# Kernel tuning notes

Measured on AMD Instinct MI355X. Metric: run time of the kernel, lower is better.

The kernel has to match this reference:

```python
import jax, jax.numpy as jnp
import numpy as np
from jax import lax

B, T, C = 4, 2048, 1024
E, DFF, TOPK = 8, 4096, 2


def setup_inputs() -> dict:
    key = jax.random.key(0)
    ks = jax.random.split(key, 5)
    scale = 0.02
    x = jax.random.normal(ks[0], (B, T, C), dtype=jnp.float32)
    router_w = jax.random.normal(ks[1], (C, E), dtype=jnp.float32) * scale
    router_b = jnp.zeros((E,), dtype=jnp.float32)
    w1 = jax.random.normal(ks[2], (E, C, DFF), dtype=jnp.float32) * scale
    b1 = jnp.zeros((E, DFF), dtype=jnp.float32)
    w2 = jax.random.normal(ks[3], (E, DFF, C), dtype=jnp.float32) * scale
    b2 = jnp.zeros((E, C), dtype=jnp.float32)
    return {"x": x, "router_w": router_w, "router_b": router_b,
            "w1": w1, "b1": b1, "w2": w2, "b2": b2, "top_k": TOPK}


def reference(x, router_w, router_b, w1, b1, w2, b2, top_k):
    # Router: softmax then top-k (matches torch.topk(F.softmax(logits)))
    logits = jnp.einsum('btc,ce->bte', x, router_w) + router_b   # [B,T,E]
    probs = jax.nn.softmax(logits, axis=-1)
    weights, indices = lax.top_k(probs, top_k)                    # [B,T,k]
    n_exp = w1.shape[0]
    # Combined per-expert weight per token (sum over top-k slots hitting expert j)
    onehot = jax.nn.one_hot(indices, n_exp, dtype=x.dtype)        # [B,T,k,E]
    cw = jnp.sum(weights[..., None] * onehot, axis=-2)            # [B,T,E]
    bsz, seq, dim = x.shape
    flat_x = x.reshape(-1, dim)                                   # [N,C]
    flat_cw = cw.reshape(-1, n_exp)                               # [N,E]
    out = jnp.zeros_like(flat_x)
    for j in range(n_exp):  # fixed small expert loop (dropout=0 -> eval)
        h = jax.nn.gelu(flat_x @ w1[j] + b1[j], approximate=False)
        out = out + flat_cw[:, j:j + 1] * (h @ w2[j] + b2[j])
    return out.reshape(bsz, seq, dim)
```

## Files before the change

### kernel.cpp

```cpp
#include <hip/hip_runtime.h>
#include <math.h>

typedef __bf16 bf16;
typedef bf16 bf16x4 __attribute__((ext_vector_type(4)));
typedef bf16 bf16x8 __attribute__((ext_vector_type(8)));
typedef float f32x4 __attribute__((ext_vector_type(4)));

#define NTOK 8192
#define CDIM 1024
#define EXP 8
#define DFF 4096
#define BM 256
#define BN 256
#define BK 64

__device__ __forceinline__ void gld_lds16(const bf16* g, bf16* l) {
  __builtin_amdgcn_global_load_lds(
      (const __attribute__((address_space(1))) unsigned int*)g,
      (__attribute__((address_space(3))) unsigned int*)l, 16, 0, 0);
}

__global__ __launch_bounds__(256) void convert_x(const float* __restrict__ in,
                                                 bf16* __restrict__ out) {
  int idx = (blockIdx.x * 256 + threadIdx.x) * 8;
  float4 a = *(const float4*)(in + idx);
  float4 b = *(const float4*)(in + idx + 4);
  bf16x8 v;
  v[0] = (bf16)a.x; v[1] = (bf16)a.y; v[2] = (bf16)a.z; v[3] = (bf16)a.w;
  v[4] = (bf16)b.x; v[5] = (bf16)b.y; v[6] = (bf16)b.z; v[7] = (bf16)b.w;
  *(bf16x8*)(out + idx) = v;
}

__global__ __launch_bounds__(256) void transpose_cvt(
    const float* __restrict__ in, bf16* __restrict__ out, int R, int Cin) {
  __shared__ float tile[32][33];
  int e = blockIdx.z;
  const float* ip = in + (size_t)e * R * Cin;
  bf16* op = out + (size_t)e * R * Cin;
  int c0 = blockIdx.x * 32, r0 = blockIdx.y * 32;
  int tx = threadIdx.x & 31, ty = threadIdx.x >> 5;
#pragma unroll
  for (int i = 0; i < 4; i++)
    tile[ty + 8 * i][tx] = ip[(size_t)(r0 + ty + 8 * i) * Cin + c0 + tx];
  __syncthreads();
  int c = threadIdx.x >> 3, r4 = (threadIdx.x & 7) * 4;
  bf16x4 v;
  v[0] = (bf16)tile[r4][c];
  v[1] = (bf16)tile[r4 + 1][c];
  v[2] = (bf16)tile[r4 + 2][c];
  v[3] = (bf16)tile[r4 + 3][c];
  *(bf16x4*)&op[(size_t)(c0 + c) * R + r0 + r4] = v;
}

__global__ __launch_bounds__(256) void router_kernel(
    const float* __restrict__ x, const float* __restrict__ rw,
    const float* __restrict__ rb, unsigned int* __restrict__ cnt,
    int* __restrict__ list, float* __restrict__ wq) {
  int wave = threadIdx.x >> 6, lane = threadIdx.x & 63;
  int t = blockIdx.x * 4 + wave;
  if (t >= NTOK) return;
  const float* xr = x + (size_t)t * CDIM;
  float acc[8] = {0.f, 0.f, 0.f, 0.f, 0.f, 0.f, 0.f, 0.f};
  for (int c = lane; c < CDIM; c += 64) {
    float xv = xr[c];
    const float4* rp = (const float4*)(rw + c * 8);
    float4 r0 = rp[0], r1 = rp[1];
    acc[0] += xv * r0.x; acc[1] += xv * r0.y;
    acc[2] += xv * r0.z; acc[3] += xv * r0.w;
    acc[4] += xv * r1.x; acc[5] += xv * r1.y;
    acc[6] += xv * r1.z; acc[7] += xv * r1.w;
  }
#pragma unroll
  for (int e = 0; e < 8; e++)
#pragma unroll
    for (int off = 32; off; off >>= 1) acc[e] += __shfl_down(acc[e], off);
  if (lane == 0) {
    float p[8], mx = -1e30f;
#pragma unroll
    for (int e = 0; e < 8; e++) { p[e] = acc[e] + rb[e]; mx = fmaxf(mx, p[e]); }
    float s = 0.f;
#pragma unroll
    for (int e = 0; e < 8; e++) { p[e] = expf(p[e] - mx); s += p[e]; }
    float inv = 1.0f / s;
#pragma unroll
    for (int e = 0; e < 8; e++) p[e] *= inv;
    int i1 = 0;
#pragma unroll
    for (int e = 1; e < 8; e++) if (p[e] > p[i1]) i1 = e;
    int i2 = (i1 == 0) ? 1 : 0;
#pragma unroll
    for (int e = 0; e < 8; e++) if (e != i1 && p[e] > p[i2]) i2 = e;
    unsigned s0 = atomicAdd(&cnt[i1], 1u);
    list[i1 * NTOK + s0] = t * 2;
    unsigned s1 = atomicAdd(&cnt[i2], 1u);
    list[i2 * NTOK + s1] = t * 2 + 1;
    wq[t * 2] = p[i1];
    wq[t * 2 + 1] = p[i2];
  }
}

__global__ __launch_bounds__(512, 2) void gemm1_kernel(
    const bf16* __restrict__ xb, const bf16* __restrict__ w1b,
    const float* __restrict__ b1, const int* __restrict__ list,
    const unsigned int* __restrict__ cnt, bf16* __restrict__ h) {
  int bid = blockIdx.x + 16 * (blockIdx.y + 32 * blockIdx.z);
  int wg = (bid & 7) * 512 + (bid >> 3);
  int n0 = (wg & 15) * BN;
  int mt = (wg >> 4) & 31;
  int e = wg >> 9;
  int count = (int)min(cnt[e], (unsigned)NTOK);
  int m0 = mt * BM;
  if (m0 >= count) return;

  __shared__ __align__(16) bf16 As[BM][BK];
  __shared__ __align__(16) bf16 Bs[BN][BK];

  int tid = threadIdx.x;
  int w = tid >> 6, l = tid & 63;
  int lhi = l >> 3, llo = l & 7;
  int w8l = w * 8 + lhi;
  int dst8 = llo * 8;
  int sc8 = (llo ^ lhi) * 8;

  const int* lp = list + e * NTOK;
  const bf16* aptr[4];
  const bf16* bptr[4];
#pragma unroll
  for (int p = 0; p < 4; p++) {
    int row = p * 64 + w8l;
    int enc = lp[min(m0 + row, count - 1)];
    aptr[p] = xb + (size_t)(enc >> 1) * CDIM + sc8;
    bptr[p] = w1b + (size_t)e * DFF * CDIM + (size_t)(n0 + row) * CDIM + sc8;
  }

  f32x4 acc[8][4] = {};
  int wm = w >> 2, wn = w & 3;
  int ln = l & 15, kq = l >> 4;
  int rx = ln & 7;

  for (int k0 = 0; k0 < CDIM; k0 += BK) {
    __syncthreads();
#pragma unroll
    for (int p = 0; p < 4; p++) {
      gld_lds16(aptr[p] + k0, &As[p * 64 + w8l][dst8]);
      gld_lds16(bptr[p] + k0, &Bs[p * 64 + w8l][dst8]);
    }
    __syncthreads();
#pragma unroll
    for (int hh = 0; hh < 2; hh++) {
      int co = ((hh * 4 + kq) ^ rx) * 8;
      bf16x8 af[8], bfr[4];
#pragma unroll
      for (int j = 0; j < 4; j++)
        bfr[j] = *(bf16x8*)&Bs[wn * 64 + j * 16 + ln][co];
#pragma unroll
      for (int i = 0; i < 8; i++)
        af[i] = *(bf16x8*)&As[wm * 128 + i * 16 + ln][co];
#pragma unroll
      for (int i = 0; i < 8; i++)
#pragma unroll
        for (int j = 0; j < 4; j++)
          acc[i][j] = __builtin_amdgcn_mfma_f32_16x16x32_bf16(
              af[i], bfr[j], acc[i][j], 0, 0, 0);
    }
  }

  float b1f[4];
#pragma unroll
  for (int j = 0; j < 4; j++)
    b1f[j] = b1[e * DFF + n0 + wn * 64 + j * 16 + ln];
#pragma unroll
  for (int i = 0; i < 8; i++) {
#pragma unroll
    for (int r = 0; r < 4; r++) {
      int mrow = wm * 128 + i * 16 + kq * 4 + r;
      if (m0 + mrow < count) {
        int enc = lp[m0 + mrow];
        bf16* hr = h + (size_t)enc * DFF + n0 + wn * 64 + ln;
#pragma unroll
        for (int j = 0; j < 4; j++) {
          float v = acc[i][j][r] + b1f[j];
          float g = 0.5f * v * (1.0f + erff(v * 0.70710678118654752f));
          hr[j * 16] = (bf16)g;
        }
      }
    }
  }
}

__global__ __launch_bounds__(512, 2) void gemm2_kernel(
    const bf16* __restrict__ h, const bf16* __restrict__ w2b,
    const float* __restrict__ b2, const int* __restrict__ list,
    const unsigned int* __restrict__ cnt, const float* __restrict__ wq,
    float* __restrict__ out) {
  int bid = blockIdx.x + 4 * (blockIdx.y + 32 * blockIdx.z);
  int wg = (bid & 7) * 128 + (bid >> 3);
  int n0 = (wg & 3) * BN;
  int mt = (wg >> 2) & 31;
  int e = wg >> 7;
  int count = (int)min(cnt[e], (unsigned)NTOK);
  int m0 = mt * BM;
  if (m0 >= count) return;

  __shared__ __align__(16) bf16 As[BM][BK];
  __shared__ __align__(16) bf16 Bs[BN][BK];

  int tid = threadIdx.x;
  int w = tid >> 6, l = tid & 63;
  int lhi = l >> 3, llo = l & 7;
  int w8l = w * 8 + lhi;
  int dst8 = llo * 8;
  int sc8 = (llo ^ lhi) * 8;

  const int* lp = list + e * NTOK;
  const bf16* aptr[4];
  const bf16* bptr[4];
#pragma unroll
  for (int p = 0; p < 4; p++) {
    int row = p * 64 + w8l;
    int enc = lp[min(m0 + row, count - 1)];
    aptr[p] = h + (size_t)enc * DFF + sc8;
    bptr[p] = w2b + (size_t)e * CDIM * DFF + (size_t)(n0 + row) * DFF + sc8;
  }

  f32x4 acc[8][4] = {};
  int wm = w >> 2, wn = w & 3;
  int ln = l & 15, kq = l >> 4;
  int rx = ln & 7;

  for (int k0 = 0; k0 < DFF; k0 += BK) {
    __syncthreads();
#pragma unroll
    for (int p = 0; p < 4; p++) {
      gld_lds16(aptr[p] + k0, &As[p * 64 + w8l][dst8]);
      gld_lds16(bptr[p] + k0, &Bs[p * 64 + w8l][dst8]);
    }
    __syncthreads();
#pragma unroll
    for (int hh = 0; hh < 2; hh++) {
      int co = ((hh * 4 + kq) ^ rx) * 8;
      bf16x8 af[8], bfr[4];
#pragma unroll
      for (int j = 0; j < 4; j++)
        bfr[j] = *(bf16x8*)&Bs[wn * 64 + j * 16 + ln][co];
#pragma unroll
      for (int i = 0; i < 8; i++)
        af[i] = *(bf16x8*)&As[wm * 128 + i * 16 + ln][co];
#pragma unroll
      for (int i = 0; i < 8; i++)
#pragma unroll
        for (int j = 0; j < 4; j++)
          acc[i][j] = __builtin_amdgcn_mfma_f32_16x16x32_bf16(
              af[i], bfr[j], acc[i][j], 0, 0, 0);
    }
  }

  float b2f[4];
#pragma unroll
  for (int j = 0; j < 4; j++)
    b2f[j] = b2[e * CDIM + n0 + wn * 64 + j * 16 + ln];
#pragma unroll
  for (int i = 0; i < 8; i++) {
#pragma unroll
    for (int r = 0; r < 4; r++) {
      int mrow = wm * 128 + i * 16 + kq * 4 + r;
      if (m0 + mrow < count) {
        int enc = lp[m0 + mrow];
        int t = enc >> 1;
        float wt = wq[enc];
        float* orow = out + (size_t)t * CDIM + n0 + wn * 64 + ln;
#pragma unroll
        for (int j = 0; j < 4; j++)
          atomicAdd(&orow[j * 16], wt * (acc[i][j][r] + b2f[j]));
      }
    }
  }
}

extern "C" void kernel_launch(void* const* d_in, const int* in_sizes, int n_in,
                              void* d_out, int out_size, void* d_ws,
                              size_t ws_size, hipStream_t stream) {
  const float* x = (const float*)d_in[0];
  const float* rw = (const float*)d_in[1];
  const float* rb = (const float*)d_in[2];
  const float* w1 = (const float*)d_in[3];
  const float* b1 = (const float*)d_in[4];
  const float* w2 = (const float*)d_in[5];
  const float* b2 = (const float*)d_in[6];
  float* out = (float*)d_out;

  char* ws = (char*)d_ws;
  size_t o = 0;
  auto carve = [&](size_t bytes) {
    void* p = ws + o;
    o = (o + bytes + 255) & ~(size_t)255;
    return p;
  };
  bf16* w1b = (bf16*)carve((size_t)EXP * DFF * CDIM * 2);
  bf16* w2b = (bf16*)carve((size_t)EXP * DFF * CDIM * 2);
  bf16* h = (bf16*)carve((size_t)2 * NTOK * DFF * 2);
  bf16* xb = (bf16*)carve((size_t)NTOK * CDIM * 2);
  int* list = (int*)carve((size_t)EXP * NTOK * 4);
  float* wq = (float*)carve((size_t)2 * NTOK * 4);
  unsigned int* cnt = (unsigned int*)carve(64);

  hipMemsetAsync(out, 0, (size_t)out_size * sizeof(float), stream);
  hipMemsetAsync(cnt, 0, 64, stream);

  convert_x<<<NTOK * CDIM / (256 * 8), 256, 0, stream>>>(x, xb);
  transpose_cvt<<<dim3(DFF / 32, CDIM / 32, EXP), 256, 0, stream>>>(w1, w1b,
                                                                    CDIM, DFF);
  transpose_cvt<<<dim3(CDIM / 32, DFF / 32, EXP), 256, 0, stream>>>(w2, w2b,
                                                                    DFF, CDIM);
  router_kernel<<<NTOK / 4, 256, 0, stream>>>(x, rw, rb, cnt, list, wq);
  gemm1_kernel<<<dim3(DFF / BN, NTOK / BM, EXP), 512, 0, stream>>>(
      xb, w1b, b1, list, cnt, h);
  gemm2_kernel<<<dim3(CDIM / BN, NTOK / BM, EXP), 512, 0, stream>>>(
      h, w2b, b2, list, cnt, wq, out);
}
```

Before: 1.202 ms.

## Pipeline grouped GEMM core with double-buffered LDS and replace atomics with combine

Replaces the two-sync GEMM main loop with a shared gemm_core that double-buffers LDS in half-K stages, issues global-to-LDS prefetches ahead of the MFMA blocks, and raises wave priority around the MFMAs, so memory latency overlaps compute. GEMM2 now writes each routed slot's weighted result to a scratch buffer (aliased onto w1b) instead of atomically adding into the output, and a new combine kernel sums the two slots per token; this also drops the output memset. The transpose kernel now handles 64-row tiles and writes 8-element vectors. The pipeline uses 128 KB of LDS per block, which may cap occupancy below the launch bound of two blocks, and the extra scratch write plus combine pass add memory traffic.

Measured after the change: 1.086 ms. 1.11x faster.

```diff
diff --git a/kernel.cpp b/kernel.cpp
--- a/kernel.cpp
+++ b/kernel.cpp
@@ -13,6 +13,7 @@
 #define BM 256
 #define BN 256
 #define BK 64
+#define HALF_E 8192
 
 __device__ __forceinline__ void gld_lds16(const bf16* g, bf16* l) {
   __builtin_amdgcn_global_load_lds(
@@ -33,23 +34,22 @@
 
 __global__ __launch_bounds__(256) void transpose_cvt(
     const float* __restrict__ in, bf16* __restrict__ out, int R, int Cin) {
-  __shared__ float tile[32][33];
+  __shared__ float tile[64][33];
   int e = blockIdx.z;
   const float* ip = in + (size_t)e * R * Cin;
   bf16* op = out + (size_t)e * R * Cin;
-  int c0 = blockIdx.x * 32, r0 = blockIdx.y * 32;
-  int tx = threadIdx.x & 31, ty = threadIdx.x >> 5;
-#pragma unroll
-  for (int i = 0; i < 4; i++)
-    tile[ty + 8 * i][tx] = ip[(size_t)(r0 + ty + 8 * i) * Cin + c0 + tx];
+  int c0 = blockIdx.x * 32, r0 = blockIdx.y * 64;
+  int tr = threadIdx.x >> 5, tc = threadIdx.x & 31;
+#pragma unroll
+  for (int i = 0; i < 8; i++)
+    tile[tr + 8 * i][tc] = ip[(size_t)(r0 + tr + 8 * i) * Cin + c0 + tc];
   __syncthreads();
-  int c = threadIdx.x >> 3, r4 = (threadIdx.x & 7) * 4;
-  bf16x4 v;
-  v[0] = (bf16)tile[r4][c];
-  v[1] = (bf16)tile[r4 + 1][c];
-  v[2] = (bf16)tile[r4 + 2][c];
-  v[3] = (bf16)tile[r4 + 3][c];
-  *(bf16x4*)&op[(size_t)(c0 + c) * R + r0 + r4] = v;
+  int oc = threadIdx.x >> 3;
+  int orr = (threadIdx.x & 7) * 8;
+  bf16x8 v;
+#pragma unroll
+  for (int k = 0; k < 8; k++) v[k] = (bf16)tile[orr + k][oc];
+  *(bf16x8*)&op[(size_t)(c0 + oc) * R + r0 + orr] = v;
 }
 
 __global__ __launch_bounds__(256) void router_kernel(
@@ -99,6 +99,108 @@
   }
 }
 
+__device__ __forceinline__ void ld_afrag(const bf16* base, int aoff, int ih,
+                                         bf16x8 (&af)[4]) {
+#pragma unroll
+  for (int i = 0; i < 4; i++)
+    af[i] = *(const bf16x8*)&base[aoff + (ih * 64 + i * 16) * 32];
+}
+__device__ __forceinline__ void ld_bfrag(const bf16* base, int boff,
+                                         bf16x8 (&bfr)[4]) {
+#pragma unroll
+  for (int j = 0; j < 4; j++)
+    bfr[j] = *(const bf16x8*)&base[boff + j * 16 * 32];
+}
+
+#define MFMA16(IH)                                                        \
+  do {                                                                    \
+    __builtin_amdgcn_s_setprio(1);                                        \
+    _Pragma("unroll") for (int i = 0; i < 4; i++)                         \
+        _Pragma("unroll") for (int j = 0; j < 4; j++) acc[(IH)*4 + i][j] = \
+            __builtin_amdgcn_mfma_f32_16x16x32_bf16(af[i], bfr[j],        \
+                                                    acc[(IH)*4 + i][j],   \
+                                                    0, 0, 0);             \
+    __builtin_amdgcn_s_setprio(0);                                        \
+  } while (0)
+
+#define STAGE(P1, P2, LDSBUF, TK, KS)                                     \
+  do {                                                                    \
+    int _k = (TK) * BK + (KS)*32;                                         \
+    bf16* _d = &LDSBUF[(((((TK)&1) << 1) | (KS)) * HALF_E) + tid * 8];    \
+    gld_lds16((P1) + _k, _d);                                             \
+    gld_lds16((P2) + _k, _d + 4096);                                      \
+  } while (0)
+
+template <int NT>
+__device__ __forceinline__ void gemm_core(
+    const bf16* aRow1, const bf16* aRow2, const bf16* bRow1, const bf16* bRow2,
+    bf16* Asf, bf16* Bsf, int tid, f32x4 (&acc)[8][4]) {
+  int w = tid >> 6, l = tid & 63;
+  int ln = l & 15, kq = l >> 4;
+  int wm = w >> 2, wn = w & 3;
+  int rc8 = (kq ^ ((ln >> 1) & 3)) * 8;
+  int aoff = (wm * 128 + ln) * 32 + rc8;
+  int boff = (wn * 64 + ln) * 32 + rc8;
+
+  bf16x8 af[4], bfr[4];
+
+  STAGE(aRow1, aRow2, Asf, 0, 0);
+  STAGE(bRow1, bRow2, Bsf, 0, 0);
+  STAGE(aRow1, aRow2, Asf, 0, 1);
+  STAGE(bRow1, bRow2, Bsf, 0, 1);
+  STAGE(aRow1, aRow2, Asf, 1, 0);
+  STAGE(bRow1, bRow2, Bsf, 1, 0);
+  asm volatile("s_waitcnt vmcnt(8)" ::: "memory");
+  __builtin_amdgcn_s_barrier();
+
+  for (int t = 0; t < NT; ++t) {
+    int sel = (t & 1) << 1;
+    const bf16* A0 = &Asf[sel * HALF_E];
+    const bf16* A1 = &Asf[(sel | 1) * HALF_E];
+    const bf16* B0 = &Bsf[sel * HALF_E];
+    const bf16* B1 = &Bsf[(sel | 1) * HALF_E];
+
+    ld_bfrag(B0, boff, bfr);
+    ld_afrag(A0, aoff, 0, af);
+    if (t + 1 < NT) STAGE(aRow1, aRow2, Asf, t + 1, 1);
+    if (t < NT - 1) asm volatile("s_waitcnt vmcnt(6)" ::: "memory");
+    else            asm volatile("s_waitcnt vmcnt(0)" ::: "memory");
+    __builtin_amdgcn_s_barrier();
+    asm volatile("s_waitcnt lgkmcnt(0)" ::: "memory");
+    __builtin_amdgcn_sched_barrier(0);
+    MFMA16(0);
+    __builtin_amdgcn_s_barrier();
+
+    ld_afrag(A0, aoff, 1, af);
+    if (t + 1 < NT) STAGE(bRow1, bRow2, Bsf, t + 1, 1);
+    __builtin_amdgcn_s_barrier();
+    asm volatile("s_waitcnt lgkmcnt(0)" ::: "memory");
+    __builtin_amdgcn_sched_barrier(0);
+    MFMA16(1);
+    __builtin_amdgcn_s_barrier();
+
+    ld_bfrag(B1, boff, bfr);
+    ld_afrag(A1, aoff, 0, af);
+    if (t + 2 < NT) STAGE(aRow1, aRow2, Asf, t + 2, 0);
+    if (t < NT - 2)       asm volatile("s_waitcnt vmcnt(6)" ::: "memory");
+    else if (t == NT - 2) asm volatile("s_waitcnt vmcnt(2)" ::: "memory");
+    else                  asm volatile("s_waitcnt vmcnt(0)" ::: "memory");
+    __builtin_amdgcn_s_barrier();
+    asm volatile("s_waitcnt lgkmcnt(0)" ::: "memory");
+    __builtin_amdgcn_sched_barrier(0);
+    MFMA16(0);
+    __builtin_amdgcn_s_barrier();
+
+    ld_afrag(A1, aoff, 1, af);
+    if (t + 2 < NT) STAGE(bRow1, bRow2, Bsf, t + 2, 0);
+    __builtin_amdgcn_s_barrier();
+    asm volatile("s_waitcnt lgkmcnt(0)" ::: "memory");
+    __builtin_amdgcn_sched_barrier(0);
+    MFMA16(1);
+    __builtin_amdgcn_s_barrier();
+  }
+}
+
 __global__ __launch_bounds__(512, 2) void gemm1_kernel(
     const bf16* __restrict__ xb, const bf16* __restrict__ w1b,
     const float* __restrict__ b1, const int* __restrict__ list,
@@ -112,59 +214,28 @@
   int m0 = mt * BM;
   if (m0 >= count) return;
 
-  __shared__ __align__(16) bf16 As[BM][BK];
-  __shared__ __align__(16) bf16 Bs[BN][BK];
+  __shared__ __align__(16) bf16 Asf[4 * HALF_E];
+  __shared__ __align__(16) bf16 Bsf[4 * HALF_E];
 
   int tid = threadIdx.x;
+  int row1 = tid >> 2;
+  int cx8 = ((tid & 3) ^ ((tid >> 3) & 3)) * 8;
+
+  const int* lp = list + e * NTOK;
+  int encA1 = lp[min(m0 + row1, count - 1)];
+  int encA2 = lp[min(m0 + row1 + 128, count - 1)];
+  const bf16* aRow1 = xb + (size_t)(encA1 >> 1) * CDIM + cx8;
+  const bf16* aRow2 = xb + (size_t)(encA2 >> 1) * CDIM + cx8;
+  const bf16* bRow1 =
+      w1b + (size_t)e * DFF * CDIM + (size_t)(n0 + row1) * CDIM + cx8;
+  const bf16* bRow2 = bRow1 + (size_t)128 * CDIM;
+
+  f32x4 acc[8][4] = {};
+  gemm_core<CDIM / BK>(aRow1, aRow2, bRow1, bRow2, Asf, Bsf, tid, acc);
+
   int w = tid >> 6, l = tid & 63;
-  int lhi = l >> 3, llo = l & 7;
-  int w8l = w * 8 + lhi;
-  int dst8 = llo * 8;
-  int sc8 = (llo ^ lhi) * 8;
-
-  const int* lp = list + e * NTOK;
-  const bf16* aptr[4];
-  const bf16* bptr[4];
-#pragma unroll
-  for (int p = 0; p < 4; p++) {
-    int row = p * 64 + w8l;
-    int enc = lp[min(m0 + row, count - 1)];
-    aptr[p] = xb + (size_t)(enc >> 1) * CDIM + sc8;
-    bptr[p] = w1b + (size_t)e * DFF * CDIM + (size_t)(n0 + row) * CDIM + sc8;
-  }
-
-  f32x4 acc[8][4] = {};
+  int ln = l & 15, kq = l >> 4;
   int wm = w >> 2, wn = w & 3;
-  int ln = l & 15, kq = l >> 4;
-  int rx = ln & 7;
-
-  for (int k0 = 0; k0 < CDIM; k0 += BK) {
-    __syncthreads();
-#pragma unroll
-    for (int p = 0; p < 4; p++) {
-      gld_lds16(aptr[p] + k0, &As[p * 64 + w8l][dst8]);
-      gld_lds16(bptr[p] + k0, &Bs[p * 64 + w8l][dst8]);
-    }
-    __syncthreads();
-#pragma unroll
-    for (int hh = 0; hh < 2; hh++) {
-      int co = ((hh * 4 + kq) ^ rx) * 8;
-      bf16x8 af[8], bfr[4];
-#pragma unroll
-      for (int j = 0; j < 4; j++)
-        bfr[j] = *(bf16x8*)&Bs[wn * 64 + j * 16 + ln][co];
-#pragma unroll
-      for (int i = 0; i < 8; i++)
-        af[i] = *(bf16x8*)&As[wm * 128 + i * 16 + ln][co];
-#pragma unroll
-      for (int i = 0; i < 8; i++)
-#pragma unroll
-        for (int j = 0; j < 4; j++)
-          acc[i][j] = __builtin_amdgcn_mfma_f32_16x16x32_bf16(
-              af[i], bfr[j], acc[i][j], 0, 0, 0);
-    }
-  }
-
   float b1f[4];
 #pragma unroll
   for (int j = 0; j < 4; j++)
@@ -192,7 +263,7 @@
     const bf16* __restrict__ h, const bf16* __restrict__ w2b,
     const float* __restrict__ b2, const int* __restrict__ list,
     const unsigned int* __restrict__ cnt, const float* __restrict__ wq,
-    float* __restrict__ out) {
+    float* __restrict__ y) {
   int bid = blockIdx.x + 4 * (blockIdx.y + 32 * blockIdx.z);
   int wg = (bid & 7) * 128 + (bid >> 3);
   int n0 = (wg & 3) * BN;
@@ -202,59 +273,28 @@
   int m0 = mt * BM;
   if (m0 >= count) return;
 
-  __shared__ __align__(16) bf16 As[BM][BK];
-  __shared__ __align__(16) bf16 Bs[BN][BK];
+  __shared__ __align__(16) bf16 Asf[4 * HALF_E];
+  __shared__ __align__(16) bf16 Bsf[4 * HALF_E];
 
   int tid = threadIdx.x;
+  int row1 = tid >> 2;
+  int cx8 = ((tid & 3) ^ ((tid >> 3) & 3)) * 8;
+
+  const int* lp = list + e * NTOK;
+  int encA1 = lp[min(m0 + row1, count - 1)];
+  int encA2 = lp[min(m0 + row1 + 128, count - 1)];
+  const bf16* aRow1 = h + (size_t)encA1 * DFF + cx8;
+  const bf16* aRow2 = h + (size_t)encA2 * DFF + cx8;
+  const bf16* bRow1 =
+      w2b + (size_t)e * CDIM * DFF + (size_t)(n0 + row1) * DFF + cx8;
+  const bf16* bRow2 = bRow1 + (size_t)128 * DFF;
+
+  f32x4 acc[8][4] = {};
+  gemm_core<DFF / BK>(aRow1, aRow2, bRow1, bRow2, Asf, Bsf, tid, acc);
+
   int w = tid >> 6, l = tid & 63;
-  int lhi = l >> 3, llo = l & 7;
-  int w8l = w * 8 + lhi;
-  int dst8 = llo * 8;
-  int sc8 = (llo ^ lhi) * 8;
-
-  const int* lp = list + e * NTOK;
-  const bf16* aptr[4];
-  const bf16* bptr[4];
-#pragma unroll
-  for (int p = 0; p < 4; p++) {
-    int row = p * 64 + w8l;
-    int enc = lp[min(m0 + row, count - 1)];
-    aptr[p] = h + (size_t)enc * DFF + sc8;
-    bptr[p] = w2b + (size_t)e * CDIM * DFF + (size_t)(n0 + row) * DFF + sc8;
-  }
-
-  f32x4 acc[8][4] = {};
+  int ln = l & 15, kq = l >> 4;
   int wm = w >> 2, wn = w & 3;
-  int ln = l & 15, kq = l >> 4;
-  int rx = ln & 7;
-
-  for (int k0 = 0; k0 < DFF; k0 += BK) {
-    __syncthreads();
-#pragma unroll
-    for (int p = 0; p < 4; p++) {
-      gld_lds16(aptr[p] + k0, &As[p * 64 + w8l][dst8]);
-      gld_lds16(bptr[p] + k0, &Bs[p * 64 + w8l][dst8]);
-    }
-    __syncthreads();
-#pragma unroll
-    for (int hh = 0; hh < 2; hh++) {
-      int co = ((hh * 4 + kq) ^ rx) * 8;
-      bf16x8 af[8], bfr[4];
-#pragma unroll
-      for (int j = 0; j < 4; j++)
-        bfr[j] = *(bf16x8*)&Bs[wn * 64 + j * 16 + ln][co];
-#pragma unroll
-      for (int i = 0; i < 8; i++)
-        af[i] = *(bf16x8*)&As[wm * 128 + i * 16 + ln][co];
-#pragma unroll
-      for (int i = 0; i < 8; i++)
-#pragma unroll
-        for (int j = 0; j < 4; j++)
-          acc[i][j] = __builtin_amdgcn_mfma_f32_16x16x32_bf16(
-              af[i], bfr[j], acc[i][j], 0, 0, 0);
-    }
-  }
-
   float b2f[4];
 #pragma unroll
   for (int j = 0; j < 4; j++)
@@ -266,15 +306,27 @@
       int mrow = wm * 128 + i * 16 + kq * 4 + r;
       if (m0 + mrow < count) {
         int enc = lp[m0 + mrow];
-        int t = enc >> 1;
         float wt = wq[enc];
-        float* orow = out + (size_t)t * CDIM + n0 + wn * 64 + ln;
+        float* yr = y + (size_t)enc * CDIM + n0 + wn * 64 + ln;
 #pragma unroll
         for (int j = 0; j < 4; j++)
-          atomicAdd(&orow[j * 16], wt * (acc[i][j][r] + b2f[j]));
+          yr[j * 16] = wt * (acc[i][j][r] + b2f[j]);
       }
     }
   }
+}
+
+__global__ __launch_bounds__(256) void combine_kernel(
+    const float* __restrict__ y, float* __restrict__ out) {
+  int idx = (blockIdx.x * 256 + threadIdx.x) * 4;
+  int t = idx >> 10;
+  int c = idx & 1023;
+  const float* y0 = y + ((size_t)(t * 2) << 10) + c;
+  float4 a = *(const float4*)y0;
+  float4 b = *(const float4*)(y0 + CDIM);
+  float4 r;
+  r.x = a.x + b.x; r.y = a.y + b.y; r.z = a.z + b.z; r.w = a.w + b.w;
+  *(float4*)(out + idx) = r;
 }
 
 extern "C" void kernel_launch(void* const* d_in, const int* in_sizes, int n_in,
@@ -303,18 +355,19 @@
   int* list = (int*)carve((size_t)EXP * NTOK * 4);
   float* wq = (float*)carve((size_t)2 * NTOK * 4);
   unsigned int* cnt = (unsigned int*)carve(64);
-
-  hipMemsetAsync(out, 0, (size_t)out_size * sizeof(float), stream);
+  float* y = (float*)w1b;
+
   hipMemsetAsync(cnt, 0, 64, stream);
 
   convert_x<<<NTOK * CDIM / (256 * 8), 256, 0, stream>>>(x, xb);
-  transpose_cvt<<<dim3(DFF / 32, CDIM / 32, EXP), 256, 0, stream>>>(w1, w1b,
+  transpose_cvt<<<dim3(DFF / 32, CDIM / 64, EXP), 256, 0, stream>>>(w1, w1b,
                                                                     CDIM, DFF);
-  transpose_cvt<<<dim3(CDIM / 32, DFF / 32, EXP), 256, 0, stream>>>(w2, w2b,
+  transpose_cvt<<<dim3(CDIM / 32, DFF / 64, EXP), 256, 0, stream>>>(w2, w2b,
                                                                     DFF, CDIM);
   router_kernel<<<NTOK / 4, 256, 0, stream>>>(x, rw, rb, cnt, list, wq);
   gemm1_kernel<<<dim3(DFF / BN, NTOK / BM, EXP), 512, 0, stream>>>(
       xb, w1b, b1, list, cnt, h);
   gemm2_kernel<<<dim3(CDIM / BN, NTOK / BM, EXP), 512, 0, stream>>>(
-      h, w2b, b2, list, cnt, wq, out);
-}
+      h, w2b, b2, list, cnt, wq, y);
+  combine_kernel<<<NTOK * CDIM / (256 * 4), 256, 0, stream>>>(y, out);
+}
```
